# Optimization experiments

Measured on AMD Instinct MI355X. Metric: run time of the kernel, lower is better.

Reference implementation:

```python
import jax, jax.numpy as jnp
import numpy as np

T, B, H, V = 256, 64, 512, 50000
SLICE = 100
NLAYERS = 2
MAX_FORGET = 0.875
HR = 23   # hidden_radix: hiddens kept in 23-bit fixed point
FR = 10   # forget-gate fixed-point radix


def _qround(x, radix):
    s = 2.0 ** radix
    return x + jax.lax.stop_gradient(jnp.round(x * s) / s - x)


def _qfloor(x, radix):
    s = 2.0 ** radix
    return x + jax.lax.stop_gradient(jnp.floor(x * s) / s - x)


def _half_update(h, z, g):
    # reversible fixed-point update: h <- floor(h * z_q) + fix((1-z)*g)
    # (remainder bits of the multiply are pushed to the InformationBuffer in
    # the original; they don't affect the forward value, only reversal)
    zq = _qfloor(z, FR)
    h = _qfloor(h * zq, HR)
    return h + _qround((1.0 - z) * g, HR)


def _cell(x, h, p):
    # RevGRU: update h1 from (x, h2), then h2 from (x, new h1)
    Wzr1, bzr1, Wg1, bg1, Wzr2, bzr2, Wg2, bg2 = p
    half = h.shape[-1] // 2
    h1, h2 = h[:, :half], h[:, half:]
    zr1 = jax.nn.sigmoid(jnp.concatenate([x, h2], -1) @ Wzr1 + bzr1)
    z1 = MAX_FORGET * zr1[:, :half] + (1.0 - MAX_FORGET)  # bounded forgetting
    r1 = zr1[:, half:]
    g1 = jnp.tanh(jnp.concatenate([x, r1 * h2], -1) @ Wg1 + bg1)
    h1 = _half_update(h1, z1, g1)
    zr2 = jax.nn.sigmoid(jnp.concatenate([x, h1], -1) @ Wzr2 + bzr2)
    z2 = MAX_FORGET * zr2[:, :half] + (1.0 - MAX_FORGET)
    r2 = zr2[:, half:]
    g2 = jnp.tanh(jnp.concatenate([x, r2 * h1], -1) @ Wg2 + bg2)
    h2 = _half_update(h2, z2, g2)
    return jnp.concatenate([h1, h2], -1)


def _forward(emb, layer_params, input_seq):
    x_seq = emb[input_seq]  # [T, B, H]
    bsz = input_seq.shape[1]
    h0 = tuple(jnp.zeros((bsz, emb.shape[1]), emb.dtype) for _ in range(NLAYERS))

    def step(carry, x):
        hs = list(carry)
        saved = hs[-1][:, :SLICE]  # top-layer slice saved BEFORE update
        cur = x
        for l in range(NLAYERS):
            hnew = _cell(cur, hs[l], layer_params[l])
            if l != NLAYERS - 1:
                cur = hnew  # output_hidden == float view of recurrent hidden
            hs[l] = hnew
        return tuple(hs), saved

    carry, saved = jax.lax.scan(step, h0, x_seq)
    saved = jnp.concatenate([saved, carry[-1][None, :, :SLICE]], 0)  # [T+1,B,slice]
    return jnp.stack(carry), saved


def setup_inputs():
    key = jax.random.key(0)
    ks = jax.random.split(key, 20)
    half = H // 2
    inp = {
        "input_seq": jax.random.randint(ks[0], (T, B), 0, V),
        "emb": jax.random.normal(ks[1], (V, H), jnp.float32) * 0.1,
    }
    i = 2
    for l in range(NLAYERS):
        for nm, (din, dout) in [("Wzr1", (H + half, H)), ("Wg1", (H + half, half)),
                                ("Wzr2", (H + half, H)), ("Wg2", (H + half, half))]:
            inp[f"{nm}_{l}"] = jax.random.normal(ks[i], (din, dout), jnp.float32) / np.sqrt(din)
            inp[f"b{nm[1:]}_{l}"] = jnp.zeros((dout,), jnp.float32)
            i += 1
    return inp


def reference(input_seq, emb,
              Wzr1_0, bzr1_0, Wg1_0, bg1_0, Wzr2_0, bzr2_0, Wg2_0, bg2_0,
              Wzr1_1, bzr1_1, Wg1_1, bg1_1, Wzr2_1, bzr2_1, Wg2_1, bg2_1):
    p0 = (Wzr1_0, bzr1_0, Wg1_0, bg1_0, Wzr2_0, bzr2_0, Wg2_0, bg2_0)
    p1 = (Wzr1_1, bzr1_1, Wg1_1, bg1_1, Wzr2_1, bzr2_1, Wg2_1, bg2_1)
    return _forward(emb, (p0, p1), input_seq)
```

## Files before the change

### kernel.cpp

```cpp
#include <hip/hip_runtime.h>
#include <hip/hip_bf16.h>
#include <stdint.h>

#define T_STEPS 256
#define BATCH   64
#define HID     512
#define HALF    256
#define NCOLS   1536
#define MROWS   (T_STEPS * BATCH)
#define SLICE_N 100
#define SAVED_OFF (2 * BATCH * HID)

#define PSLOT 2048
#define PSTEP (12 * PSLOT)

#define RING_D 32
#define NHELP 24

#define XBUF 16384
#define WG_FRAGS 6144

typedef short bf16x8 __attribute__((ext_vector_type(8)));
typedef float f32x4  __attribute__((ext_vector_type(4)));

__device__ __forceinline__ f32x4 mfma16(bf16x8 a, bf16x8 b, f32x4 c) {
  return __builtin_amdgcn_mfma_f32_16x16x32_bf16(a, b, c, 0, 0, 0);
}
__device__ __forceinline__ float sigm_f(float x) {
  return __builtin_amdgcn_rcpf(1.f + __expf(-x));
}
__device__ __forceinline__ float tanh_f(float x) {
  x = fminf(fmaxf(x, -30.f), 30.f);
  float e = __expf(-2.f * x);
  return (1.f - e) * __builtin_amdgcn_rcpf(1.f + e);
}

__device__ __forceinline__ unsigned long long coh_u64(const void* p) {
  return __hip_atomic_load((const unsigned long long*)p, __ATOMIC_RELAXED,
                           __HIP_MEMORY_SCOPE_AGENT);
}
__device__ __forceinline__ void coh_store_u64(void* p, unsigned long long v) {
  __hip_atomic_store((unsigned long long*)p, v, __ATOMIC_RELAXED,
                     __HIP_MEMORY_SCOPE_AGENT);
}
__device__ __forceinline__ bf16x8 coh_frag(const void* p) {
  union { unsigned long long u[2]; bf16x8 v; } x;
  x.u[0] = coh_u64(p);
  x.u[1] = coh_u64((const char*)p + 8);
  return x.v;
}
__device__ __forceinline__ float4 coh_f4(const void* p) {
  union { unsigned long long u[2]; float4 v; } x;
  x.u[0] = coh_u64(p);
  x.u[1] = coh_u64((const char*)p + 8);
  return x.v;
}

#define POLLGE(addr, val)                                                        \
  while (__hip_atomic_load((addr), __ATOMIC_RELAXED, __HIP_MEMORY_SCOPE_AGENT) < \
         (uint32_t)(val))                                                        \
    __builtin_amdgcn_s_sleep(1);

#define CFENCE() asm volatile("" ::: "memory")

struct AllW {
  const float* W[8];
  const float* b[8];
};

__global__ void prep_weights(AllW aw, __hip_bfloat16* __restrict__ Wcs,
                             __hip_bfloat16* __restrict__ WxT,
                             float* __restrict__ biasAll,
                             uint32_t* __restrict__ flags) {
  int tid = blockIdx.x * blockDim.x + threadIdx.x;
  if (tid < 4096) flags[tid] = 0u;
  const int NWc = 2 * 8 * WG_FRAGS;
  const int NX = 2 * NCOLS * 64;
  if (tid < NWc) {
    int l = tid / (8 * WG_FRAGS), r = tid % (8 * WG_FRAGS);
    int j = r / WG_FRAGS, r2 = r % WG_FRAGS;
    int g = r2 >> 6, lane = r2 & 63;
    int lrow = lane & 15, lgrp = lane >> 4;
    int s, gg;
    if (g < 32)      { s = 0; gg = g; }
    else if (g < 48) { s = 1; gg = g - 32; }
    else if (g < 80) { s = 2; gg = g - 48; }
    else             { s = 3; gg = g - 80; }
    int ct = gg >> 3, kt = gg & 7;
    int zr = (s == 0 || s == 2);
    int nc = zr ? 512 : 256;
    int cb = zr ? (ct < 2 ? 32 * j + 16 * ct : 256 + 32 * j + 16 * (ct - 2))
                : (32 * j + 16 * ct);
    const float* W = aw.W[l * 4 + s];
    int kbase = 512 + kt * 32 + lgrp * 8;
    __hip_bfloat16 frag[8];
#pragma unroll
    for (int e = 0; e < 8; ++e)
      frag[e] = __float2bfloat16(W[(size_t)(kbase + e) * nc + cb + lrow]);
    *(uint4*)&Wcs[(size_t)tid * 8] = *(uint4*)frag;
  } else if (tid < NWc + NX) {
    int u = tid - NWc;
    int l = u / (NCOLS * 64), r = u % (NCOLS * 64);
    int c = r >> 6, k0 = (r & 63) * 8;
    const float* W; int nc, cc;
    if (c < 512)       { W = aw.W[l*4+0]; nc = 512; cc = c;        }
    else if (c < 768)  { W = aw.W[l*4+1]; nc = 256; cc = c - 512;  }
    else if (c < 1280) { W = aw.W[l*4+2]; nc = 512; cc = c - 768;  }
    else               { W = aw.W[l*4+3]; nc = 256; cc = c - 1280; }
    __hip_bfloat16 frag[8];
#pragma unroll
    for (int e = 0; e < 8; ++e)
      frag[e] = __float2bfloat16(W[(size_t)(k0 + e) * nc + cc]);
    *(uint4*)&WxT[((size_t)l * NCOLS + c) * 512 + k0] = *(uint4*)frag;
  } else if (tid < NWc + NX + 2 * NCOLS) {
    int c = tid - NWc - NX;
    int l = c / NCOLS, cc = c % NCOLS;
    const float* b; int off;
    if (cc < 512)       { b = aw.b[l*4+0]; off = cc;        }
    else if (cc < 768)  { b = aw.b[l*4+1]; off = cc - 512;  }
    else if (cc < 1280) { b = aw.b[l*4+2]; off = cc - 768;  }
    else                { b = aw.b[l*4+3]; off = cc - 1280; }
    biasAll[c] = b[off];
  }
}

__global__ void embed_gather(const int* __restrict__ seq, const float* __restrict__ emb,
                             __hip_bfloat16* __restrict__ X0) {
  int i = blockIdx.x * blockDim.x + threadIdx.x;
  int row = i >> 7, c4 = (i & 127) * 4;
  int idx = seq[row];
  float4 v = *(const float4*)&emb[(size_t)idx * HID + c4];
  union { __hip_bfloat16 h[4]; uint2 u; } pk;
  pk.h[0] = __float2bfloat16(v.x);
  pk.h[1] = __float2bfloat16(v.y);
  pk.h[2] = __float2bfloat16(v.z);
  pk.h[3] = __float2bfloat16(v.w);
  *(uint2*)&X0[(size_t)row * HID + c4] = pk.u;
}

__global__ __launch_bounds__(256) void gemm_p(const __hip_bfloat16* __restrict__ A,
                                              const __hip_bfloat16* __restrict__ WT,
                                              const float* __restrict__ bias,
                                              float* __restrict__ Psw) {
  const int tid = threadIdx.x;
  const int lane = tid & 63, w = tid >> 6;
  const int lrow = lane & 15, lgrp = lane >> 4;
  const int n0 = blockIdx.x * 64, m0 = blockIdx.y * 64;
  const int wm = w & 1, wn = w >> 1;
  __shared__ __hip_bfloat16 As[64][72];
  f32x4 acc[2][2];
#pragma unroll
  for (int a = 0; a < 2; ++a)
#pragma unroll
    for (int b = 0; b < 2; ++b) acc[a][b] = (f32x4){0.f, 0.f, 0.f, 0.f};

  const int lr = tid >> 2, lc = (tid & 3) * 16;
  for (int k0 = 0; k0 < 512; k0 += 64) {
    *(uint4*)&As[lr][lc]     = *(const uint4*)&A[((size_t)m0 + lr) * 512 + k0 + lc];
    *(uint4*)&As[lr][lc + 8] = *(const uint4*)&A[((size_t)m0 + lr) * 512 + k0 + lc + 8];
    __syncthreads();
#pragma unroll
    for (int kt = 0; kt < 2; ++kt) {
      bf16x8 a0 = *(const bf16x8*)&As[wm * 32 + lrow][kt * 32 + lgrp * 8];
      bf16x8 a1 = *(const bf16x8*)&As[wm * 32 + 16 + lrow][kt * 32 + lgrp * 8];
      bf16x8 b0 = *(const bf16x8*)&WT[((size_t)n0 + wn * 32 + lrow) * 512 + k0 + kt * 32 + lgrp * 8];
      bf16x8 b1 = *(const bf16x8*)&WT[((size_t)n0 + wn * 32 + 16 + lrow) * 512 + k0 + kt * 32 + lgrp * 8];
      acc[0][0] = mfma16(a0, b0, acc[0][0]);
      acc[0][1] = mfma16(a0, b1, acc[0][1]);
      acc[1][0] = mfma16(a1, b0, acc[1][0]);
      acc[1][1] = mfma16(a1, b1, acc[1][1]);
    }
    __syncthreads();
  }
  const int t = m0 >> 6;
#pragma unroll
  for (int mt = 0; mt < 2; ++mt) {
    int g = wm * 2 + mt;
#pragma unroll
    for (int nt = 0; nt < 2; ++nt) {
      int colb = n0 + wn * 32 + nt * 16;
      int slot, wt;
      if (colb < 512)       { int c = colb;        wt = (c & 255) >> 5; slot = (c >> 8) * 2 + ((c >> 4) & 1); }
      else if (colb < 768)  { int c = colb - 512;  wt = c >> 5;         slot = 4 + ((c >> 4) & 1); }
      else if (colb < 1280) { int c = colb - 768;  wt = (c & 255) >> 5; slot = 6 + (c >> 8) * 2 + ((c >> 4) & 1); }
      else                  { int c = colb - 1280; wt = c >> 5;         slot = 10 + ((c >> 4) & 1); }
      float bv = bias[colb + lrow];
      float4 v;
      v.x = acc[mt][nt][0] + bv;
      v.y = acc[mt][nt][1] + bv;
      v.z = acc[mt][nt][2] + bv;
      v.w = acc[mt][nt][3] + bv;
      size_t off = (((size_t)g * 256 + t) * 12 + slot) * PSLOT + (size_t)wt * 256 + (size_t)lane * 4;
      *(float4*)&Psw[off] = v;
    }
  }
}

struct SharedMem {
  union {
    struct {
      __hip_bfloat16 Wl[WG_FRAGS * 8];
      __hip_bfloat16 Ab[XBUF];
      __hip_bfloat16 st[2048];
      float zl[2048];
      float h1s[2048];
      float h2s[2048];
    } rec;
    struct {
      __hip_bfloat16 Bs[64][520];
      __hip_bfloat16 As[2 * XBUF];
      float bias[64];
    } hlp;
  };
};

template <int LAYER>
__device__ __forceinline__ const float* paddr(const float* Pb, int g4, int t,
                                              int slot, int j, int lane) {
  size_t tt = LAYER ? (size_t)(t & (RING_D - 1)) : (size_t)t;
  size_t TD = LAYER ? RING_D : 256;
  return Pb + (((size_t)g4 * TD + tt) * 12 + slot) * PSLOT + (size_t)j * 256 +
         (size_t)lane * 4;
}

#define AB_FILL(srcbuf)                                                      \
  {                                                                          \
    const char* sp = (const char*)(srcbuf) + (size_t)tid * 16;               \
    bf16x8 t0 = coh_frag(sp);                                                \
    bf16x8 t1 = coh_frag(sp + 8192);                                         \
    bf16x8 t2 = coh_frag(sp + 16384);                                        \
    bf16x8 t3 = coh_frag(sp + 24576);                                        \
    *(bf16x8*)&Ab[((size_t)0 * 512 + tid) * 8] = t0;                         \
    *(bf16x8*)&Ab[((size_t)1 * 512 + tid) * 8] = t1;                         \
    *(bf16x8*)&Ab[((size_t)2 * 512 + tid) * 8] = t2;                         \
    *(bf16x8*)&Ab[((size_t)3 * 512 + tid) * 8] = t3;                         \
  }

template <int LAYER>
__device__ void rec_body(const __hip_bfloat16* __restrict__ Wcs_j,
                         const float* __restrict__ Pbase,
                         __hip_bfloat16* __restrict__ R,
                         float* __restrict__ out,
                         uint32_t* __restrict__ flags,
                         SharedMem& sm, int j) {
  const int tid = threadIdx.x;
  const int lane = tid & 63, w = tid >> 6;
  const int lrow = lane & 15, lgrp = lane >> 4;

  uint32_t* F = flags + LAYER * 1024;
  uint32_t* cnt1 = flags + 2048;
  uint32_t* l1prog = flags + 2304;

  __hip_bfloat16* const Wl = sm.rec.Wl;
  __hip_bfloat16* const Ab = sm.rec.Ab;
  __hip_bfloat16* const st = sm.rec.st;
  float* const zl  = sm.rec.zl;
  float* const h1s = sm.rec.h1s;
  float* const h2s = sm.rec.h2s;

  const int HM = LAYER ? 1 : 7;
  __hip_bfloat16* const h1r = R + (size_t)(LAYER ? 20 : 0)  * XBUF;
  __hip_bfloat16* const h2r = R + (size_t)(LAYER ? 22 : 8)  * XBUF;
  __hip_bfloat16* const ag1 = R + (size_t)(LAYER ? 24 : 16) * XBUF;
  __hip_bfloat16* const ag2 = R + (size_t)(LAYER ? 26 : 18) * XBUF;

  for (int i = tid; i < WG_FRAGS; i += 512)
    *(bf16x8*)&Wl[(size_t)i * 8] = *(const bf16x8*)&Wcs_j[(size_t)i * 8];
  for (int i = tid; i < 2048; i += 512) { h1s[i] = 0.f; h2s[i] = 0.f; }
  if (LAYER == 1)
    for (int i = tid; i < 64 * 32; i += 512) {
      int row = i >> 5, c = 32 * j + (i & 31);
      if (c < SLICE_N) out[SAVED_OFF + (size_t)row * SLICE_N + c] = 0.f;
    }
  __syncthreads();

  const int ct13 = w >> 1, a0 = (w & 1) * 2, a1 = a0 + 1;
  const int cl13 = 16 * (ct13 & 1) + lrow;
  const int lt13 = (lgrp * 4) | ((cl13 >> 3) << 4);
  const int el13 = cl13 & 7;
  const int ct24 = w >> 2, a24 = w & 3;
  const int cl24 = 16 * ct24 + lrow;
  const int lt24 = (lgrp * 4) | ((cl24 >> 3) << 4);
  const int el24 = cl24 & 7;
  const int col24 = 32 * j + cl24;
  const int row24 = a24 * 16 + lgrp * 4;
  const int pu = lane >> 1, phf = (lane & 1) * 4;
  const int plt13 = (ct13 & 1) * 32 + pu;
  const int plt24 = ct24 * 32 + pu;

  const float Q23 = 8388608.f, IQ23 = 1.f / 8388608.f;
  const float Q10 = 1024.f,    IQ10 = 1.f / 1024.f;

  float hr1[4] = {0.f, 0.f, 0.f, 0.f};
  float hr2[4] = {0.f, 0.f, 0.f, 0.f};

  for (int t = 0; t < T_STEPS; ++t) {
    auto LDP = [&](int g, int slot) -> float4 {
      const float* a = paddr<LAYER>(Pbase, g, t, slot, j, lane);
      if (LAYER == 1) return coh_f4(a);
      return *(const float4*)a;
    };
    float4 P_s1_0, P_s1_1, P_s2, P_s3_0, P_s3_1, P_s4;
    if (LAYER == 0) {
      P_s1_0 = LDP(a0, ct13);      P_s1_1 = LDP(a1, ct13);
      P_s2   = LDP(a24, 4 + ct24);
      P_s3_0 = LDP(a0, 6 + ct13);  P_s3_1 = LDP(a1, 6 + ct13);
      P_s4   = LDP(a24, 10 + ct24);
    }

    if (tid == 0) {
      if (LAYER == 1) { POLLGE(&cnt1[t], NHELP); }
      if (t > 0)      { POLLGE(&F[3 * 256 + t - 1], 8); }
    }
    __syncthreads();
    if (LAYER == 1) {
      P_s1_0 = LDP(a0, ct13);      P_s1_1 = LDP(a1, ct13);
      P_s2   = LDP(a24, 4 + ct24);
      P_s3_0 = LDP(a0, 6 + ct13);  P_s3_1 = LDP(a1, 6 + ct13);
      P_s4   = LDP(a24, 10 + ct24);
    }
    if (t == 0) {
      bf16x8 zz = {0, 0, 0, 0, 0, 0, 0, 0};
#pragma unroll
      for (int q = 0; q < 4; ++q) *(bf16x8*)&Ab[((size_t)q * 512 + tid) * 8] = zz;
    } else {
      AB_FILL(&h2r[(size_t)((t - 1) & HM) * XBUF]);
    }
    __syncthreads();
    {
      f32x4 c0 = (f32x4){0.f, 0.f, 0.f, 0.f}, c1 = c0;
#pragma unroll
      for (int kt = 0; kt < 8; ++kt) {
        bf16x8 A0 = *(const bf16x8*)&Ab[((a0 * 8 + kt) * 64 + lane) * 8];
        bf16x8 A1 = *(const bf16x8*)&Ab[((a1 * 8 + kt) * 64 + lane) * 8];
        bf16x8 B  = *(const bf16x8*)&Wl[((ct13 * 8 + kt) * 64 + lane) * 8];
        c0 = mfma16(A0, B, c0);
        c1 = mfma16(A1, B, c1);
      }
      if (ct13 < 2) {
#pragma unroll
        for (int rr = 0; rr < 4; ++rr) {
          zl[(a0 * 16 + lgrp * 4 + rr) * 32 + cl13] = 0.875f * sigm_f(c0[rr] + P_s1_0[rr]) + 0.125f;
          zl[(a1 * 16 + lgrp * 4 + rr) * 32 + cl13] = 0.875f * sigm_f(c1[rr] + P_s1_1[rr]) + 0.125f;
        }
      } else {
#pragma unroll
        for (int rr = 0; rr < 4; ++rr) {
          float r0 = sigm_f(c0[rr] + P_s1_0[rr]);
          float r1 = sigm_f(c1[rr] + P_s1_1[rr]);
          st[(a0 * 64 + lt13 + rr) * 8 + el13] =
              __float2bfloat16(r0 * h2s[(a0 * 16 + lgrp * 4 + rr) * 32 + cl13]);
          st[(a1 * 64 + lt13 + rr) * 8 + el13] =
              __float2bfloat16(r1 * h2s[(a1 * 16 + lgrp * 4 + rr) * 32 + cl13]);
        }
        CFENCE();
        __hip_bfloat16* dst = &ag1[(size_t)(t & 1) * XBUF];
        unsigned long long v0 = *(const unsigned long long*)&st[(a0 * 64 + plt13) * 8 + phf];
        unsigned long long v1 = *(const unsigned long long*)&st[(a1 * 64 + plt13) * 8 + phf];
        coh_store_u64(&dst[((size_t)(a0 * 8 + j) * 64 + plt13) * 8 + phf], v0);
        coh_store_u64(&dst[((size_t)(a1 * 8 + j) * 64 + plt13) * 8 + phf], v1);
      }
    }
    __syncthreads();
    if (tid == 0)
      __hip_atomic_fetch_add(&F[0 * 256 + t], 1u, __ATOMIC_RELAXED, __HIP_MEMORY_SCOPE_AGENT);

    if (tid == 0) {
      POLLGE(&F[0 * 256 + t], 8);
      if (LAYER == 0 && t >= 8) { POLLGE(&cnt1[t - 8], NHELP); }
    }
    __syncthreads();
    AB_FILL(&ag1[(size_t)(t & 1) * XBUF]);
    __syncthreads();
    {
      f32x4 c = (f32x4){0.f, 0.f, 0.f, 0.f};
#pragma unroll
      for (int kt = 0; kt < 8; ++kt) {
        bf16x8 A = *(const bf16x8*)&Ab[((a24 * 8 + kt) * 64 + lane) * 8];
        bf16x8 B = *(const bf16x8*)&Wl[((32 + ct24 * 8 + kt) * 64 + lane) * 8];
        c = mfma16(A, B, c);
      }
#pragma unroll
      for (int rr = 0; rr < 4; ++rr) {
        float gv = tanh_f(c[rr] + P_s2[rr]);
        float z  = zl[(row24 + rr) * 32 + cl24];
        float zq = floorf(z * Q10) * IQ10;
        float h = hr1[rr];
        h = floorf(h * zq * Q23) * IQ23;
        h = h + rintf((1.f - z) * gv * Q23) * IQ23;
        hr1[rr] = h;
        h1s[(row24 + rr) * 32 + cl24] = h;
        st[(a24 * 64 + lt24 + rr) * 8 + el24] = __float2bfloat16(h);
        int row = row24 + rr;
        if (LAYER == 1 && col24 < SLICE_N)
          out[SAVED_OFF + (size_t)(t + 1) * (BATCH * SLICE_N) + (size_t)row * SLICE_N + col24] = h;
        if (t == T_STEPS - 1)
          out[(size_t)LAYER * (BATCH * HID) + (size_t)row * HID + col24] = h;
      }
      CFENCE();
      __hip_bfloat16* dst = &h1r[(size_t)(t & HM) * XBUF];
      unsigned long long v = *(const unsigned long long*)&st[(a24 * 64 + plt24) * 8 + phf];
      coh_store_u64(&dst[((size_t)(a24 * 8 + j) * 64 + plt24) * 8 + phf], v);
    }
    __syncthreads();
    if (tid == 0)
      __hip_atomic_fetch_add(&F[1 * 256 + t], 1u, __ATOMIC_RELAXED, __HIP_MEMORY_SCOPE_AGENT);

    if (tid == 0) { POLLGE(&F[1 * 256 + t], 8); }
    __syncthreads();
    AB_FILL(&h1r[(size_t)(t & HM) * XBUF]);
    __syncthreads();
    {
      f32x4 c0 = (f32x4){0.f, 0.f, 0.f, 0.f}, c1 = c0;
#pragma unroll
      for (int kt = 0; kt < 8; ++kt) {
        bf16x8 A0 = *(const bf16x8*)&Ab[((a0 * 8 + kt) * 64 + lane) * 8];
        bf16x8 A1 = *(const bf16x8*)&Ab[((a1 * 8 + kt) * 64 + lane) * 8];
        bf16x8 B  = *(const bf16x8*)&Wl[((48 + ct13 * 8 + kt) * 64 + lane) * 8];
        c0 = mfma16(A0, B, c0);
        c1 = mfma16(A1, B, c1);
      }
      if (ct13 < 2) {
#pragma unroll
        for (int rr = 0; rr < 4; ++rr) {
          zl[(a0 * 16 + lgrp * 4 + rr) * 32 + cl13] = 0.875f * sigm_f(c0[rr] + P_s3_0[rr]) + 0.125f;
          zl[(a1 * 16 + lgrp * 4 + rr) * 32 + cl13] = 0.875f * sigm_f(c1[rr] + P_s3_1[rr]) + 0.125f;
        }
      } else {
#pragma unroll
        for (int rr = 0; rr < 4; ++rr) {
          float r0 = sigm_f(c0[rr] + P_s3_0[rr]);
          float r1 = sigm_f(c1[rr] + P_s3_1[rr]);
          st[(a0 * 64 + lt13 + rr) * 8 + el13] =
              __float2bfloat16(r0 * h1s[(a0 * 16 + lgrp * 4 + rr) * 32 + cl13]);
          st[(a1 * 64 + lt13 + rr) * 8 + el13] =
              __float2bfloat16(r1 * h1s[(a1 * 16 + lgrp * 4 + rr) * 32 + cl13]);
        }
        CFENCE();
        __hip_bfloat16* dst = &ag2[(size_t)(t & 1) * XBUF];
        unsigned long long v0 = *(const unsigned long long*)&st[(a0 * 64 + plt13) * 8 + phf];
        unsigned long long v1 = *(const unsigned long long*)&st[(a1 * 64 + plt13) * 8 + phf];
        coh_store_u64(&dst[((size_t)(a0 * 8 + j) * 64 + plt13) * 8 + phf], v0);
        coh_store_u64(&dst[((size_t)(a1 * 8 + j) * 64 + plt13) * 8 + phf], v1);
      }
    }
    __syncthreads();
    if (tid == 0)
      __hip_atomic_fetch_add(&F[2 * 256 + t], 1u, __ATOMIC_RELAXED, __HIP_MEMORY_SCOPE_AGENT);

    if (tid == 0) { POLLGE(&F[2 * 256 + t], 8); }
    __syncthreads();
    AB_FILL(&ag2[(size_t)(t & 1) * XBUF]);
    __syncthreads();
    {
      f32x4 c = (f32x4){0.f, 0.f, 0.f, 0.f};
#pragma unroll
      for (int kt = 0; kt < 8; ++kt) {
        bf16x8 A = *(const bf16x8*)&Ab[((a24 * 8 + kt) * 64 + lane) * 8];
        bf16x8 B = *(const bf16x8*)&Wl[((80 + ct24 * 8 + kt) * 64 + lane) * 8];
        c = mfma16(A, B, c);
      }
#pragma unroll
      for (int rr = 0; rr < 4; ++rr) {
        float gv = tanh_f(c[rr] + P_s4[rr]);
        float z  = zl[(row24 + rr) * 32 + cl24];
        float zq = floorf(z * Q10) * IQ10;
        float h = hr2[rr];
        h = floorf(h * zq * Q23) * IQ23;
        h = h + rintf((1.f - z) * gv * Q23) * IQ23;
        hr2[rr] = h;
        h2s[(row24 + rr) * 32 + cl24] = h;
        st[(a24 * 64 + lt24 + rr) * 8 + el24] = __float2bfloat16(h);
        int row = row24 + rr;
        if (t == T_STEPS - 1)
          out[(size_t)LAYER * (BATCH * HID) + (size_t)row * HID + HALF + col24] = h;
      }
      CFENCE();
      __hip_bfloat16* dst = &h2r[(size_t)(t & HM) * XBUF];
      unsigned long long v = *(const unsigned long long*)&st[(a24 * 64 + plt24) * 8 + phf];
      coh_store_u64(&dst[((size_t)(a24 * 8 + j) * 64 + plt24) * 8 + phf], v);
    }
    __syncthreads();
    if (tid == 0) {
      __hip_atomic_fetch_add(&F[3 * 256 + t], 1u, __ATOMIC_RELAXED, __HIP_MEMORY_SCOPE_AGENT);
      if (LAYER == 1)
        __hip_atomic_store(&l1prog[j], (uint32_t)(t + 1), __ATOMIC_RELAXED, __HIP_MEMORY_SCOPE_AGENT);
    }
  }
}

__device__ void helper_body(const __hip_bfloat16* __restrict__ WxT1,
                            const float* __restrict__ bias1,
                            const __hip_bfloat16* __restrict__ R,
                            float* __restrict__ P1ring,
                            uint32_t* __restrict__ flags,
                            SharedMem& sm, int n) {
  const int tid = threadIdx.x;
  const int lane = tid & 63, w = tid >> 6;
  const int lrow = lane & 15, lgrp = lane >> 4;
  const int n0 = n * 64;

  uint32_t* F0 = flags;
  uint32_t* cnt1 = flags + 2048;
  uint32_t* l1prog = flags + 2304;
  const __hip_bfloat16* h1r = R;
  const __hip_bfloat16* h2r = R + (size_t)8 * XBUF;

  for (int i = tid; i < 64 * 64; i += 512) {
    int c = i >> 6, k8 = (i & 63) * 8;
    *(bf16x8*)&sm.hlp.Bs[c][k8] = *(const bf16x8*)&WxT1[(size_t)(n0 + c) * 512 + k8];
  }
  if (tid < 64) sm.hlp.bias[tid] = bias1[n0 + tid];
  __syncthreads();

  const int mt = w & 3, chb = (w >> 2) * 2;

  for (int t = 0; t < T_STEPS; ++t) {
    if (tid == 0) {
      POLLGE(&F0[3 * 256 + t], 8);
      if (t >= RING_D) {
        for (;;) {
          uint32_t mm = 0xffffffffu;
#pragma unroll
          for (int q = 0; q < 8; ++q) {
            uint32_t v = __hip_atomic_load(&l1prog[q], __ATOMIC_RELAXED, __HIP_MEMORY_SCOPE_AGENT);
            mm = v < mm ? v : mm;
          }
          if (mm + (uint32_t)(RING_D - 1) >= (uint32_t)t) break;
          __builtin_amdgcn_s_sleep(1);
        }
      }
    }
    __syncthreads();
    {
      const char* s1 = (const char*)&h1r[(size_t)(t & 7) * XBUF] + (size_t)tid * 16;
      const char* s2 = (const char*)&h2r[(size_t)(t & 7) * XBUF] + (size_t)tid * 16;
      bf16x8 tA[8];
#pragma unroll
      for (int k = 0; k < 4; ++k) tA[k] = coh_frag(s1 + (size_t)k * 8192);
#pragma unroll
      for (int k = 4; k < 8; ++k) tA[k] = coh_frag(s2 + (size_t)(k - 4) * 8192);
#pragma unroll
      for (int k = 0; k < 8; ++k) *(bf16x8*)&sm.hlp.As[(size_t)(k * 512 + tid) * 8] = tA[k];
    }
    __syncthreads();
#pragma unroll
    for (int q = 0; q < 2; ++q) {
      int ch = chb + q;
      f32x4 c = (f32x4){0.f, 0.f, 0.f, 0.f};
#pragma unroll
      for (int kt = 0; kt < 16; ++kt) {
        const bf16x8 A = *(const bf16x8*)&sm.hlp.As[
            kt < 8 ? (size_t)((mt * 8 + kt) * 64 + lane) * 8
                   : (size_t)XBUF + (size_t)((mt * 8 + (kt - 8)) * 64 + lane) * 8];
        const bf16x8 B = *(const bf16x8*)&sm.hlp.Bs[ch * 16 + lrow][kt * 32 + lgrp * 8];
        c = mfma16(A, B, c);
      }
      int colb = n0 + ch * 16;
      int slot, wt;
      if (colb < 512)       { int cc = colb;        wt = (cc & 255) >> 5; slot = (cc >> 8) * 2 + ((cc >> 4) & 1); }
      else if (colb < 768)  { int cc = colb - 512;  wt = cc >> 5;         slot = 4 + ((cc >> 4) & 1); }
      else if (colb < 1280) { int cc = colb - 768;  wt = (cc & 255) >> 5; slot = 6 + (cc >> 8) * 2 + ((cc >> 4) & 1); }
      else                  { int cc = colb - 1280; wt = cc >> 5;         slot = 10 + ((cc >> 4) & 1); }
      float bv = sm.hlp.bias[ch * 16 + lrow];
      union { float4 f; unsigned long long u[2]; } uv;
      uv.f.x = c[0] + bv; uv.f.y = c[1] + bv; uv.f.z = c[2] + bv; uv.f.w = c[3] + bv;
      size_t off = (((size_t)mt * RING_D + (t & (RING_D - 1))) * 12 + slot) * PSLOT +
                   (size_t)wt * 256 + (size_t)lane * 4;
      unsigned long long* d = (unsigned long long*)&P1ring[off];
      coh_store_u64(d, uv.u[0]);
      coh_store_u64(d + 1, uv.u[1]);
    }
    __syncthreads();
    if (tid == 0)
      __hip_atomic_fetch_add(&cnt1[t], 1u, __ATOMIC_RELAXED, __HIP_MEMORY_SCOPE_AGENT);
  }
}

__global__ __attribute__((amdgpu_waves_per_eu(2))) __launch_bounds__(512)
void fused_kernel(const __hip_bfloat16* __restrict__ Wcs,
                  const float* __restrict__ Psw0,
                  float* __restrict__ P1ring,
                  const __hip_bfloat16* __restrict__ WxT1,
                  const float* __restrict__ bias1,
                  float* __restrict__ out,
                  __hip_bfloat16* __restrict__ R,
                  uint32_t* __restrict__ flags) {
  __shared__ SharedMem sm;
  const int bid = blockIdx.x;
  if (bid < 8)
    rec_body<0>(Wcs + (size_t)bid * WG_FRAGS * 8, Psw0, R, out, flags, sm, bid);
  else if (bid < 16)
    rec_body<1>(Wcs + (size_t)(8 + (bid - 8)) * WG_FRAGS * 8, P1ring, R, out, flags, sm, bid - 8);
  else
    helper_body(WxT1, bias1, R, P1ring, flags, sm, bid - 16);
}

extern "C" void kernel_launch(void* const* d_in, const int* in_sizes, int n_in,
                              void* d_out, int out_size, void* d_ws, size_t ws_size,
                              hipStream_t stream) {
  const int*   seq = (const int*)d_in[0];
  const float* emb = (const float*)d_in[1];
  AllW aw;
  for (int l = 0; l < 2; ++l)
    for (int s = 0; s < 4; ++s) {
      aw.W[l * 4 + s] = (const float*)d_in[2 + l * 8 + s * 2];
      aw.b[l * 4 + s] = (const float*)d_in[2 + l * 8 + s * 2 + 1];
    }

  uint8_t* wp = (uint8_t*)d_ws;
  float* Psw = (float*)wp;                   wp += (size_t)4 * 256 * PSTEP * 4;
  __hip_bfloat16* X0 = (__hip_bfloat16*)wp;  wp += (size_t)MROWS * HID * 2;
  __hip_bfloat16* R  = (__hip_bfloat16*)wp;  wp += (size_t)MROWS * HID * 2;
  __hip_bfloat16* Wcs = (__hip_bfloat16*)wp; wp += (size_t)2 * 8 * WG_FRAGS * 8 * 2;
  __hip_bfloat16* WxT = (__hip_bfloat16*)wp; wp += (size_t)2 * NCOLS * 512 * 2;
  float* biasAll = (float*)wp;               wp += (size_t)2 * NCOLS * 4;
  uint32_t* flags = (uint32_t*)wp;           wp += 16384;

  float* out = (float*)d_out;

  const int prepTot = 2 * 8 * WG_FRAGS + 2 * NCOLS * 64 + 2 * NCOLS;
  const int prepN = (prepTot + 255) / 256;
  prep_weights<<<prepN, 256, 0, stream>>>(aw, Wcs, WxT, biasAll, flags);
  embed_gather<<<(MROWS * 128) / 256, 256, 0, stream>>>(seq, emb, X0);

  gemm_p<<<dim3(24, 256), 256, 0, stream>>>(X0, WxT, biasAll, Psw);
  fused_kernel<<<8 + 8 + NHELP, 512, 0, stream>>>(
      Wcs, Psw, (float*)X0, WxT + (size_t)NCOLS * 512, biasAll + NCOLS,
      out, R, flags);
}
```

Before: 3.030 ms.

## Co-locate recurrent blocks on one XCD and sync via local L2 flags

Launches 64 blocks with block index mod 8 chosen so each layer's eight recurrent workgroups are likely to land on the same XCD. The kernel detects whether that happened by reading the XCC id register, and if so switches to a fast mode. Fast mode uses non-coherent stores, L2-scoped atomic flags and L1 invalidates in place of device-coherent loads and stores for the intra-layer exchanges. It also moves the layer-0 throttle poll to the start of each step. This should cut cross-die synchronization latency per step, at the cost of depending on the hardware's block-to-XCD placement and on hand-written inline-asm cache semantics being correct.

```diff
diff --git a/kernel.cpp b/kernel.cpp
--- a/kernel.cpp
+++ b/kernel.cpp
@@ -61,6 +61,23 @@
          (uint32_t)(val))                                                        \
     __builtin_amdgcn_s_sleep(1);
 
+__device__ __forceinline__ void l2_flag_add(uint32_t* p) {
+  uint32_t one = 1u;
+  asm volatile("global_atomic_add %0, %1, off" :: "v"(p), "v"(one) : "memory");
+}
+__device__ __forceinline__ uint32_t l2_flag_read(uint32_t* p) {
+  uint32_t r, zero = 0u;
+  asm volatile("global_atomic_add %0, %1, %2, off sc0\n\t"
+               "s_waitcnt vmcnt(0)"
+               : "=&v"(r) : "v"(p), "v"(zero) : "memory");
+  return r;
+}
+#define L2POLLGE(addr, val)                                                  \
+  while (l2_flag_read(addr) < (uint32_t)(val)) __builtin_amdgcn_s_sleep(1);
+__device__ __forceinline__ void l1_inv() {
+  asm volatile("buffer_inv sc0\n\ts_waitcnt vmcnt(0)" ::: "memory");
+}
+
 #define CFENCE() asm volatile("" ::: "memory")
 
 struct AllW {
@@ -73,7 +90,7 @@
                              float* __restrict__ biasAll,
                              uint32_t* __restrict__ flags) {
   int tid = blockIdx.x * blockDim.x + threadIdx.x;
-  if (tid < 4096) flags[tid] = 0u;
+  if (tid < 8192) flags[tid] = 0u;
   const int NWc = 2 * 8 * WG_FRAGS;
   const int NX = 2 * NCOLS * 64;
   if (tid < NWc) {
@@ -205,6 +222,7 @@
       float zl[2048];
       float h1s[2048];
       float h2s[2048];
+      uint32_t fastf;
     } rec;
     struct {
       __hip_bfloat16 Bs[64][520];
@@ -223,17 +241,25 @@
          (size_t)lane * 4;
 }
 
-#define AB_FILL(srcbuf)                                                      \
+#define AB_FILL_ANY(srcbuf, FMF)                                             \
   {                                                                          \
-    const char* sp = (const char*)(srcbuf) + (size_t)tid * 16;               \
-    bf16x8 t0 = coh_frag(sp);                                                \
-    bf16x8 t1 = coh_frag(sp + 8192);                                         \
-    bf16x8 t2 = coh_frag(sp + 16384);                                        \
-    bf16x8 t3 = coh_frag(sp + 24576);                                        \
-    *(bf16x8*)&Ab[((size_t)0 * 512 + tid) * 8] = t0;                         \
-    *(bf16x8*)&Ab[((size_t)1 * 512 + tid) * 8] = t1;                         \
-    *(bf16x8*)&Ab[((size_t)2 * 512 + tid) * 8] = t2;                         \
-    *(bf16x8*)&Ab[((size_t)3 * 512 + tid) * 8] = t3;                         \
+    const char* sp_ = (const char*)(srcbuf) + (size_t)tid * 16;              \
+    bf16x8 t0_, t1_, t2_, t3_;                                               \
+    if (FMF) {                                                               \
+      t0_ = *(const bf16x8*)(sp_);                                           \
+      t1_ = *(const bf16x8*)(sp_ + 8192);                                    \
+      t2_ = *(const bf16x8*)(sp_ + 16384);                                   \
+      t3_ = *(const bf16x8*)(sp_ + 24576);                                   \
+    } else {                                                                 \
+      t0_ = coh_frag(sp_);                                                   \
+      t1_ = coh_frag(sp_ + 8192);                                            \
+      t2_ = coh_frag(sp_ + 16384);                                           \
+      t3_ = coh_frag(sp_ + 24576);                                           \
+    }                                                                        \
+    *(bf16x8*)&Ab[((size_t)0 * 512 + tid) * 8] = t0_;                        \
+    *(bf16x8*)&Ab[((size_t)1 * 512 + tid) * 8] = t1_;                        \
+    *(bf16x8*)&Ab[((size_t)2 * 512 + tid) * 8] = t2_;                        \
+    *(bf16x8*)&Ab[((size_t)3 * 512 + tid) * 8] = t3_;                        \
   }
 
 template <int LAYER>
@@ -250,6 +276,9 @@
   uint32_t* F = flags + LAYER * 1024;
   uint32_t* cnt1 = flags + 2048;
   uint32_t* l1prog = flags + 2304;
+  uint32_t* xccb = flags + 2560;
+  uint32_t* xcnt = flags + 2592;
+  uint32_t* Fl = flags + 4096 + LAYER * 1024;
 
   __hip_bfloat16* const Wl = sm.rec.Wl;
   __hip_bfloat16* const Ab = sm.rec.Ab;
@@ -263,6 +292,20 @@
   __hip_bfloat16* const h2r = R + (size_t)(LAYER ? 22 : 8)  * XBUF;
   __hip_bfloat16* const ag1 = R + (size_t)(LAYER ? 24 : 16) * XBUF;
   __hip_bfloat16* const ag2 = R + (size_t)(LAYER ? 26 : 18) * XBUF;
+  __hip_bfloat16* const Lb  = R + (size_t)(32 + LAYER * 8) * XBUF;
+  __hip_bfloat16* const lag1 = Lb + 0 * XBUF;
+  __hip_bfloat16* const lag2 = Lb + 2 * XBUF;
+  __hip_bfloat16* const lh1  = Lb + 4 * XBUF;
+  __hip_bfloat16* const lh2  = Lb + 6 * XBUF;
+
+  if (tid == 0) {
+    uint32_t xcc;
+    asm volatile("s_getreg_b32 %0, hwreg(20, 0, 32)" : "=s"(xcc));
+    __hip_atomic_store(&xccb[LAYER * 8 + j], (xcc & 15u) | 256u,
+                       __ATOMIC_RELAXED, __HIP_MEMORY_SCOPE_AGENT);
+    asm volatile("s_waitcnt vmcnt(0)" ::: "memory");
+    __hip_atomic_fetch_add(&xcnt[LAYER], 1u, __ATOMIC_RELAXED, __HIP_MEMORY_SCOPE_AGENT);
+  }
 
   for (int i = tid; i < WG_FRAGS; i += 512)
     *(bf16x8*)&Wl[(size_t)i * 8] = *(const bf16x8*)&Wcs_j[(size_t)i * 8];
@@ -273,6 +316,17 @@
       if (c < SLICE_N) out[SAVED_OFF + (size_t)row * SLICE_N + c] = 0.f;
     }
   __syncthreads();
+  if (tid == 0) {
+    POLLGE(&xcnt[LAYER], 8);
+    uint32_t v0 = __hip_atomic_load(&xccb[LAYER * 8], __ATOMIC_RELAXED, __HIP_MEMORY_SCOPE_AGENT);
+    uint32_t same = 1;
+    for (int q = 1; q < 8; ++q)
+      same &= (__hip_atomic_load(&xccb[LAYER * 8 + q], __ATOMIC_RELAXED,
+                                 __HIP_MEMORY_SCOPE_AGENT) == v0) ? 1u : 0u;
+    sm.rec.fastf = same;
+  }
+  __syncthreads();
+  const bool FM = (sm.rec.fastf != 0);
 
   const int ct13 = w >> 1, a0 = (w & 1) * 2, a1 = a0 + 1;
   const int cl13 = 16 * (ct13 & 1) + lrow;
@@ -287,6 +341,12 @@
   const int pu = lane >> 1, phf = (lane & 1) * 4;
   const int plt13 = (ct13 & 1) * 32 + pu;
   const int plt24 = ct24 * 32 + pu;
+  const size_t go13a = ((size_t)(a0 * 8 + j) * 64 + plt13) * 8 + phf;
+  const size_t go13b = ((size_t)(a1 * 8 + j) * 64 + plt13) * 8 + phf;
+  const size_t go24  = ((size_t)(a24 * 8 + j) * 64 + plt24) * 8 + phf;
+  const size_t so13a = (size_t)(a0 * 64 + plt13) * 8 + phf;
+  const size_t so13b = (size_t)(a1 * 64 + plt13) * 8 + phf;
+  const size_t so24  = (size_t)(a24 * 64 + plt24) * 8 + phf;
 
   const float Q23 = 8388608.f, IQ23 = 1.f / 8388608.f;
   const float Q10 = 1024.f,    IQ10 = 1.f / 1024.f;
@@ -310,9 +370,14 @@
 
     if (tid == 0) {
       if (LAYER == 1) { POLLGE(&cnt1[t], NHELP); }
-      if (t > 0)      { POLLGE(&F[3 * 256 + t - 1], 8); }
-    }
-    __syncthreads();
+      if (LAYER == 0 && t >= 8) { POLLGE(&cnt1[t - 8], NHELP); }
+      if (t > 0) {
+        if (FM) { L2POLLGE(&Fl[3 * 256 + t - 1], 8); }
+        else    { POLLGE(&F[3 * 256 + t - 1], 8); }
+      }
+    }
+    __syncthreads();
+    if (FM) l1_inv();
     if (LAYER == 1) {
       P_s1_0 = LDP(a0, ct13);      P_s1_1 = LDP(a1, ct13);
       P_s2   = LDP(a24, 4 + ct24);
@@ -324,7 +389,9 @@
 #pragma unroll
       for (int q = 0; q < 4; ++q) *(bf16x8*)&Ab[((size_t)q * 512 + tid) * 8] = zz;
     } else {
-      AB_FILL(&h2r[(size_t)((t - 1) & HM) * XBUF]);
+      const __hip_bfloat16* src = FM ? (lh2 + (size_t)((t - 1) & 1) * XBUF)
+                                     : (h2r + (size_t)((t - 1) & HM) * XBUF);
+      AB_FILL_ANY(src, FM);
     }
     __syncthreads();
     {
@@ -354,23 +421,34 @@
               __float2bfloat16(r1 * h2s[(a1 * 16 + lgrp * 4 + rr) * 32 + cl13]);
         }
         CFENCE();
-        __hip_bfloat16* dst = &ag1[(size_t)(t & 1) * XBUF];
-        unsigned long long v0 = *(const unsigned long long*)&st[(a0 * 64 + plt13) * 8 + phf];
-        unsigned long long v1 = *(const unsigned long long*)&st[(a1 * 64 + plt13) * 8 + phf];
-        coh_store_u64(&dst[((size_t)(a0 * 8 + j) * 64 + plt13) * 8 + phf], v0);
-        coh_store_u64(&dst[((size_t)(a1 * 8 + j) * 64 + plt13) * 8 + phf], v1);
-      }
-    }
-    __syncthreads();
-    if (tid == 0)
-      __hip_atomic_fetch_add(&F[0 * 256 + t], 1u, __ATOMIC_RELAXED, __HIP_MEMORY_SCOPE_AGENT);
-
-    if (tid == 0) {
-      POLLGE(&F[0 * 256 + t], 8);
-      if (LAYER == 0 && t >= 8) { POLLGE(&cnt1[t - 8], NHELP); }
-    }
-    __syncthreads();
-    AB_FILL(&ag1[(size_t)(t & 1) * XBUF]);
+        unsigned long long v0 = *(const unsigned long long*)&st[so13a];
+        unsigned long long v1 = *(const unsigned long long*)&st[so13b];
+        __hip_bfloat16* dst = (FM ? lag1 : ag1) + (size_t)(t & 1) * XBUF;
+        if (FM) {
+          *(unsigned long long*)&dst[go13a] = v0;
+          *(unsigned long long*)&dst[go13b] = v1;
+        } else {
+          coh_store_u64(&dst[go13a], v0);
+          coh_store_u64(&dst[go13b], v1);
+        }
+      }
+    }
+    __syncthreads();
+    if (tid == 0) {
+      if (FM) l2_flag_add(&Fl[0 * 256 + t]);
+      else __hip_atomic_fetch_add(&F[0 * 256 + t], 1u, __ATOMIC_RELAXED, __HIP_MEMORY_SCOPE_AGENT);
+    }
+
+    if (tid == 0) {
+      if (FM) { L2POLLGE(&Fl[0 * 256 + t], 8); }
+      else    { POLLGE(&F[0 * 256 + t], 8); }
+    }
+    __syncthreads();
+    if (FM) l1_inv();
+    {
+      const __hip_bfloat16* src = (FM ? lag1 : ag1) + (size_t)(t & 1) * XBUF;
+      AB_FILL_ANY(src, FM);
+    }
     __syncthreads();
     {
       f32x4 c = (f32x4){0.f, 0.f, 0.f, 0.f};
@@ -398,17 +476,32 @@
           out[(size_t)LAYER * (BATCH * HID) + (size_t)row * HID + col24] = h;
       }
       CFENCE();
-      __hip_bfloat16* dst = &h1r[(size_t)(t & HM) * XBUF];
-      unsigned long long v = *(const unsigned long long*)&st[(a24 * 64 + plt24) * 8 + phf];
-      coh_store_u64(&dst[((size_t)(a24 * 8 + j) * 64 + plt24) * 8 + phf], v);
-    }
-    __syncthreads();
-    if (tid == 0)
-      __hip_atomic_fetch_add(&F[1 * 256 + t], 1u, __ATOMIC_RELAXED, __HIP_MEMORY_SCOPE_AGENT);
-
-    if (tid == 0) { POLLGE(&F[1 * 256 + t], 8); }
-    __syncthreads();
-    AB_FILL(&h1r[(size_t)(t & HM) * XBUF]);
+      unsigned long long v = *(const unsigned long long*)&st[so24];
+      if (FM) {
+        *(unsigned long long*)&(lh1 + (size_t)(t & 1) * XBUF)[go24] = v;
+        if (LAYER == 0)
+          coh_store_u64(&(h1r + (size_t)(t & 7) * XBUF)[go24], v);
+      } else {
+        coh_store_u64(&(h1r + (size_t)(t & HM) * XBUF)[go24], v);
+      }
+    }
+    __syncthreads();
+    if (tid == 0) {
+      if (FM) l2_flag_add(&Fl[1 * 256 + t]);
+      else __hip_atomic_fetch_add(&F[1 * 256 + t], 1u, __ATOMIC_RELAXED, __HIP_MEMORY_SCOPE_AGENT);
+    }
+
+    if (tid == 0) {
+      if (FM) { L2POLLGE(&Fl[1 * 256 + t], 8); }
+      else    { POLLGE(&F[1 * 256 + t], 8); }
+    }
+    __syncthreads();
+    if (FM) l1_inv();
+    {
+      const __hip_bfloat16* src = FM ? (lh1 + (size_t)(t & 1) * XBUF)
+                                     : (h1r + (size_t)(t & HM) * XBUF);
+      AB_FILL_ANY(src, FM);
+    }
     __syncthreads();
     {
       f32x4 c0 = (f32x4){0.f, 0.f, 0.f, 0.f}, c1 = c0;
@@ -437,20 +530,34 @@
               __float2bfloat16(r1 * h1s[(a1 * 16 + lgrp * 4 + rr) * 32 + cl13]);
         }
         CFENCE();
-        __hip_bfloat16* dst = &ag2[(size_t)(t & 1) * XBUF];
-        unsigned long long v0 = *(const unsigned long long*)&st[(a0 * 64 + plt13) * 8 + phf];
-        unsigned long long v1 = *(const unsigned long long*)&st[(a1 * 64 + plt13) * 8 + phf];
-        coh_store_u64(&dst[((size_t)(a0 * 8 + j) * 64 + plt13) * 8 + phf], v0);
-        coh_store_u64(&dst[((size_t)(a1 * 8 + j) * 64 + plt13) * 8 + phf], v1);
-      }
-    }
-    __syncthreads();
-    if (tid == 0)
-      __hip_atomic_fetch_add(&F[2 * 256 + t], 1u, __ATOMIC_RELAXED, __HIP_MEMORY_SCOPE_AGENT);
-
-    if (tid == 0) { POLLGE(&F[2 * 256 + t], 8); }
-    __syncthreads();
-    AB_FILL(&ag2[(size_t)(t & 1) * XBUF]);
+        unsigned long long v0 = *(const unsigned long long*)&st[so13a];
+        unsigned long long v1 = *(const unsigned long long*)&st[so13b];
+        __hip_bfloat16* dst = (FM ? lag2 : ag2) + (size_t)(t & 1) * XBUF;
+        if (FM) {
+          *(unsigned long long*)&dst[go13a] = v0;
+          *(unsigned long long*)&dst[go13b] = v1;
+        } else {
+          coh_store_u64(&dst[go13a], v0);
+          coh_store_u64(&dst[go13b], v1);
+        }
+      }
+    }
+    __syncthreads();
+    if (tid == 0) {
+      if (FM) l2_flag_add(&Fl[2 * 256 + t]);
+      else __hip_atomic_fetch_add(&F[2 * 256 + t], 1u, __ATOMIC_RELAXED, __HIP_MEMORY_SCOPE_AGENT);
+    }
+
+    if (tid == 0) {
+      if (FM) { L2POLLGE(&Fl[2 * 256 + t], 8); }
+      else    { POLLGE(&F[2 * 256 + t], 8); }
+    }
+    __syncthreads();
+    if (FM) l1_inv();
+    {
+      const __hip_bfloat16* src = (FM ? lag2 : ag2) + (size_t)(t & 1) * XBUF;
+      AB_FILL_ANY(src, FM);
+    }
     __syncthreads();
     {
       f32x4 c = (f32x4){0.f, 0.f, 0.f, 0.f};
@@ -476,15 +583,28 @@
           out[(size_t)LAYER * (BATCH * HID) + (size_t)row * HID + HALF + col24] = h;
       }
       CFENCE();
-      __hip_bfloat16* dst = &h2r[(size_t)(t & HM) * XBUF];
-      unsigned long long v = *(const unsigned long long*)&st[(a24 * 64 + plt24) * 8 + phf];
-      coh_store_u64(&dst[((size_t)(a24 * 8 + j) * 64 + plt24) * 8 + phf], v);
-    }
-    __syncthreads();
-    if (tid == 0) {
-      __hip_atomic_fetch_add(&F[3 * 256 + t], 1u, __ATOMIC_RELAXED, __HIP_MEMORY_SCOPE_AGENT);
-      if (LAYER == 1)
-        __hip_atomic_store(&l1prog[j], (uint32_t)(t + 1), __ATOMIC_RELAXED, __HIP_MEMORY_SCOPE_AGENT);
+      unsigned long long v = *(const unsigned long long*)&st[so24];
+      if (FM) {
+        *(unsigned long long*)&(lh2 + (size_t)(t & 1) * XBUF)[go24] = v;
+        if (LAYER == 0)
+          coh_store_u64(&(h2r + (size_t)(t & 7) * XBUF)[go24], v);
+      } else {
+        coh_store_u64(&(h2r + (size_t)(t & HM) * XBUF)[go24], v);
+      }
+    }
+    __syncthreads();
+    if (tid == 0) {
+      if (FM) {
+        l2_flag_add(&Fl[3 * 256 + t]);
+        if (LAYER == 0)
+          __hip_atomic_fetch_add(&F[3 * 256 + t], 1u, __ATOMIC_RELAXED, __HIP_MEMORY_SCOPE_AGENT);
+        if (LAYER == 1)
+          __hip_atomic_store(&l1prog[j], (uint32_t)(t + 1), __ATOMIC_RELAXED, __HIP_MEMORY_SCOPE_AGENT);
+      } else {
+        __hip_atomic_fetch_add(&F[3 * 256 + t], 1u, __ATOMIC_RELAXED, __HIP_MEMORY_SCOPE_AGENT);
+        if (LAYER == 1)
+          __hip_atomic_store(&l1prog[j], (uint32_t)(t + 1), __ATOMIC_RELAXED, __HIP_MEMORY_SCOPE_AGENT);
+      }
     }
   }
 }
@@ -588,12 +708,13 @@
                   uint32_t* __restrict__ flags) {
   __shared__ SharedMem sm;
   const int bid = blockIdx.x;
-  if (bid < 8)
-    rec_body<0>(Wcs + (size_t)bid * WG_FRAGS * 8, Psw0, R, out, flags, sm, bid);
-  else if (bid < 16)
-    rec_body<1>(Wcs + (size_t)(8 + (bid - 8)) * WG_FRAGS * 8, P1ring, R, out, flags, sm, bid - 8);
-  else
-    helper_body(WxT1, bias1, R, P1ring, flags, sm, bid - 16);
+  const int xslot = bid & 7, idx = bid >> 3;
+  if (xslot == 0)
+    rec_body<0>(Wcs + (size_t)idx * WG_FRAGS * 8, Psw0, R, out, flags, sm, idx);
+  else if (xslot == 1)
+    rec_body<1>(Wcs + (size_t)(8 + idx) * WG_FRAGS * 8, P1ring, R, out, flags, sm, idx);
+  else if (idx < 4)
+    helper_body(WxT1, bias1, R, P1ring, flags, sm, (xslot - 2) * 4 + idx);
 }
 
 extern "C" void kernel_launch(void* const* d_in, const int* in_sizes, int n_in,
@@ -615,7 +736,7 @@
   __hip_bfloat16* Wcs = (__hip_bfloat16*)wp; wp += (size_t)2 * 8 * WG_FRAGS * 8 * 2;
   __hip_bfloat16* WxT = (__hip_bfloat16*)wp; wp += (size_t)2 * NCOLS * 512 * 2;
   float* biasAll = (float*)wp;               wp += (size_t)2 * NCOLS * 4;
-  uint32_t* flags = (uint32_t*)wp;           wp += 16384;
+  uint32_t* flags = (uint32_t*)wp;           wp += 32768;
 
   float* out = (float*)d_out;
 
@@ -625,7 +746,7 @@
   embed_gather<<<(MROWS * 128) / 256, 256, 0, stream>>>(seq, emb, X0);
 
   gemm_p<<<dim3(24, 256), 256, 0, stream>>>(X0, WxT, biasAll, Psw);
-  fused_kernel<<<8 + 8 + NHELP, 512, 0, stream>>>(
+  fused_kernel<<<64, 512, 0, stream>>>(
       Wcs, Psw, (float*)X0, WxT + (size_t)NCOLS * 512, biasAll + NCOLS,
       out, R, flags);
 }
```

After: 2.505 ms. 1.21x faster.
